# Kernel tuning notes

Hardware: AMD Instinct MI355X
Metric: run time of the kernel (lower is better)

The kernel has to match this reference:

```python
import jax, jax.numpy as jnp
import numpy as np

DIM, E, H, HS = 2048, 8, 1408, 2816
B, S = 4, 2048


def setup_inputs() -> dict:
    key = jax.random.key(0)
    ks = jax.random.split(key, 12)
    sc = 0.02
    return {
        "x": jax.random.normal(ks[0], (B, S, DIM), jnp.float32),
        "gate_w": jax.random.normal(ks[1], (E, DIM), jnp.float32) * sc,
        "gate_b": jnp.zeros((E,), jnp.float32),
        "w1": jax.random.normal(ks[2], (E, H, DIM), jnp.float32) * sc,
        "b1": jnp.zeros((E, H), jnp.float32),
        "w3": jax.random.normal(ks[3], (E, H, DIM), jnp.float32) * sc,
        "b3": jnp.zeros((E, H), jnp.float32),
        "w2": jax.random.normal(ks[4], (E, DIM, H), jnp.float32) * sc,
        "b2": jnp.zeros((E, DIM), jnp.float32),
        "sh_gate": jax.random.normal(ks[5], (HS, DIM), jnp.float32) * sc,
        "sh_up": jax.random.normal(ks[6], (HS, DIM), jnp.float32) * sc,
        "sh_down": jax.random.normal(ks[7], (DIM, HS), jnp.float32) * sc,
        "top_k": 2,
    }


def reference(x, gate_w, gate_b, w1, b1, w3, b3, w2, b2, sh_gate, sh_up, sh_down, top_k):
    shape = x.shape
    xt = x.reshape(-1, DIM)                       # [T, D]
    T = xt.shape[0]

    # Router: softmax -> top-k (bias is None so gathered weights == topk probs)
    logits = xt @ gate_w.T + gate_b               # [T, E]
    scores = jax.nn.softmax(logits, axis=-1)
    topk_w, topk_idx = jax.lax.top_k(scores, top_k)  # [T, K]
    # combine weights per (token, expert); topk indices are distinct per row
    combine = jnp.zeros((T, E), xt.dtype).at[jnp.arange(T)[:, None], topk_idx].add(topk_w)

    # Routed experts: dense batched SwiGLU over all experts, weighted combine.
    g = jax.nn.silu(jnp.einsum("td,ehd->teh", xt, w1) + b1)  # [T, E, H]
    u = jnp.einsum("td,ehd->teh", xt, w3) + b3               # [T, E, H]
    hw = (g * u) * combine[:, :, None]                        # weight before down-proj
    routed = jnp.einsum("teh,edh->td", hw, w2) + combine @ b2  # [T, D]

    # Shared expert (bias-free SwiGLU)
    shared = (jax.nn.silu(xt @ sh_gate.T) * (xt @ sh_up.T)) @ sh_down.T

    return (shared + routed).reshape(shape)
```

## Files before the change

### kernel.cpp

```cpp
#include <hip/hip_runtime.h>
#include <stdint.h>

#define DIM  2048
#define NEXP 8
#define NH   1408
#define NHS  2816
#define NT   8192
#define NA   (NT*2)

typedef unsigned short u16;
typedef short bf16x8 __attribute__((ext_vector_type(8)));
typedef float f32x4 __attribute__((ext_vector_type(4)));

typedef __attribute__((address_space(1))) const uint32_t gas_u32;
typedef __attribute__((address_space(3))) uint32_t las_u32;

__device__ __forceinline__ u16 f2bf(float f) {
  uint32_t x = __builtin_bit_cast(uint32_t, f);
  x += 0x7FFFu + ((x >> 16) & 1u);
  return (u16)(x >> 16);
}

__device__ __forceinline__ void gload_lds16(const void* g, void* l) {
  __builtin_amdgcn_global_load_lds((gas_u32*)g, (las_u32*)l, 16, 0, 0);
}

__device__ __forceinline__ bool xcd_map_band(int G, int& nt, int& mt) {
  const int gx = gridDim.x;
  int f = blockIdx.y * gx + blockIdx.x;
  int xcd = f & 7;
  int local = f >> 3;
  if (G <= 0) return false;
  int band = (G + 7) >> 3;
  int slot = local % band;
  int ntv  = local / band;
  if (ntv >= gx) return false;
  int mtv = xcd * band + slot;
  if (mtv >= G) return false;
  nt = ntv; mt = mtv;
  return true;
}

struct alignas(16) US8 { u16 u[8]; };
struct alignas(8)  US4 { u16 u[4]; };

__global__ __launch_bounds__(256) void convert_kernel(const float* __restrict__ src,
                                                      u16* __restrict__ dst, int n8) {
  int i = blockIdx.x * 256 + threadIdx.x;
  if (i >= n8) return;
  const float4* s = (const float4*)src + (size_t)i * 2;
  float4 a = s[0], b = s[1];
  US8 r;
  r.u[0]=f2bf(a.x); r.u[1]=f2bf(a.y); r.u[2]=f2bf(a.z); r.u[3]=f2bf(a.w);
  r.u[4]=f2bf(b.x); r.u[5]=f2bf(b.y); r.u[6]=f2bf(b.z); r.u[7]=f2bf(b.w);
  *((US8*)dst + i) = r;
}

__global__ void zero_counts(int* counts) { if (threadIdx.x < NEXP) counts[threadIdx.x] = 0; }

__global__ __launch_bounds__(64) void router_kernel(const float* __restrict__ x,
    const float* __restrict__ gw, const float* __restrict__ gb,
    u16* __restrict__ xb,
    int* __restrict__ tope, float* __restrict__ topw, int* __restrict__ counts) {
  const int t = blockIdx.x;
  const int lane = threadIdx.x;
  const float4* xr = (const float4*)(x + (size_t)t * DIM);
  float4 xv[8];
  #pragma unroll
  for (int j = 0; j < 8; j++) xv[j] = xr[j * 64 + lane];
  US4* xrow = (US4*)(xb + (size_t)t * DIM);
  #pragma unroll
  for (int j = 0; j < 8; j++) {
    US4 r4;
    r4.u[0] = f2bf(xv[j].x); r4.u[1] = f2bf(xv[j].y);
    r4.u[2] = f2bf(xv[j].z); r4.u[3] = f2bf(xv[j].w);
    xrow[j * 64 + lane] = r4;
  }
  float p[NEXP];
  #pragma unroll
  for (int e = 0; e < NEXP; e++) {
    const float4* gr = (const float4*)(gw + (size_t)e * DIM);
    float s = 0.f;
    #pragma unroll
    for (int j = 0; j < 8; j++) {
      float4 g = gr[j * 64 + lane];
      s += xv[j].x*g.x + xv[j].y*g.y + xv[j].z*g.z + xv[j].w*g.w;
    }
    p[e] = s;
  }
  #pragma unroll
  for (int off = 32; off > 0; off >>= 1) {
    #pragma unroll
    for (int e = 0; e < NEXP; e++) p[e] += __shfl_xor(p[e], off);
  }
  if (lane == 0) {
    float pr[NEXP];
    float mx = -1e30f;
    #pragma unroll
    for (int e = 0; e < NEXP; e++) { p[e] += gb[e]; mx = fmaxf(mx, p[e]); }
    float den = 0.f;
    #pragma unroll
    for (int e = 0; e < NEXP; e++) { pr[e] = __expf(p[e] - mx); den += pr[e]; }
    float inv = 1.f / den;
    #pragma unroll
    for (int e = 0; e < NEXP; e++) pr[e] *= inv;
    int e0 = 0;
    #pragma unroll
    for (int e = 1; e < NEXP; e++) if (pr[e] > pr[e0]) e0 = e;
    int e1 = (e0 == 0) ? 1 : 0;
    #pragma unroll
    for (int e = 0; e < NEXP; e++) { if (e != e0 && pr[e] > pr[e1]) e1 = e; }
    tope[t*2]   = e0; tope[t*2+1] = e1;
    topw[t*2]   = pr[e0]; topw[t*2+1] = pr[e1];
    atomicAdd(&counts[e0], 1); atomicAdd(&counts[e1], 1);
  }
}

__global__ void scan_kernel(const int* __restrict__ counts, int* __restrict__ offsets,
                            int* __restrict__ cursor) {
  if (threadIdx.x == 0) {
    int s = 0;
    for (int e = 0; e < NEXP; e++) { offsets[e] = s; cursor[e] = s; s += counts[e]; }
    offsets[NEXP] = s;
  }
}

__global__ __launch_bounds__(256) void assign_kernel(const int* __restrict__ tope,
    const float* __restrict__ topw, int* __restrict__ cursor,
    int* __restrict__ ptok, float* __restrict__ pw) {
  int t = blockIdx.x * 256 + threadIdx.x;
  if (t >= NT) return;
  #pragma unroll
  for (int k = 0; k < 2; k++) {
    int e = tope[t*2+k];
    int pos = atomicAdd(&cursor[e], 1);
    ptok[pos] = t;
    pw[pos]   = topw[t*2+k];
  }
}

template<bool ROUTED>
__global__ __launch_bounds__(256, 2) void gemm_up(
    const u16* __restrict__ X,
    const u16* __restrict__ Wg,
    const u16* __restrict__ Wu,
    const float* __restrict__ Bg,
    const float* __restrict__ Bu,
    u16* __restrict__ Hout,
    const int* __restrict__ offsets,
    const int* __restrict__ ptok,
    const float* __restrict__ pw,
    int Nfeat)
{
  int e = 0, seg = 0, cnt = NT;
  if (ROUTED) {
    e = blockIdx.z;
    seg = offsets[e];
    cnt = offsets[e+1] - seg;
  }
  const int G = ROUTED ? ((cnt + 127) >> 7) : (int)gridDim.y;
  int nt, mt;
  if (!xcd_map_band(G, nt, mt)) return;
  const int m0 = mt * 128;
  const int tid = threadIdx.x;
  const int wave = tid >> 6, lane = tid & 63;

  __shared__ u16 sA[128*64];
  __shared__ u16 sBg[64*64];
  __shared__ u16 sBu[64*64];
  char* sAc  = (char*)sA;
  char* sBgc = (char*)sBg;
  char* sBuc = (char*)sBu;

  const u16* aSrc[4];
  #pragma unroll
  for (int j = 0; j < 4; j++) {
    int c = j * 256 + tid;
    int row = c >> 3, gch = (c & 7) ^ (row & 7);
    int r = m0 + row;
    size_t srow;
    if (ROUTED) { r = (r < cnt) ? r : (cnt - 1); srow = (size_t)ptok[seg + r]; }
    else        { srow = (size_t)r; }
    aSrc[j] = X + srow * DIM + gch * 8;
  }
  const size_t wOff = ROUTED ? (size_t)e * Nfeat * DIM : 0;
  const u16 *bgSrc[2], *buSrc[2];
  #pragma unroll
  for (int j = 0; j < 2; j++) {
    int c = j * 256 + tid;
    int row = c >> 3, gch = (c & 7) ^ (row & 7);
    bgSrc[j] = Wg + wOff + (size_t)(nt * 64 + row) * DIM + gch * 8;
    buSrc[j] = Wu + wOff + (size_t)(nt * 64 + row) * DIM + gch * 8;
  }

  f32x4 accg[4][2], accu[4][2];
  #pragma unroll
  for (int m = 0; m < 4; m++)
    #pragma unroll
    for (int n = 0; n < 2; n++) { accg[m][n] = (f32x4){0,0,0,0}; accu[m][n] = (f32x4){0,0,0,0}; }

  const int wr = (wave >> 1) * 64;
  const int wc = (wave & 1) * 32;
  const int lr = lane & 15, kg = lane >> 4;
  int aOff[4], bOff[2];
  #pragma unroll
  for (int m = 0; m < 4; m++) { int row = wr + m*16 + lr; aOff[m] = row*128 + ((kg ^ (row & 7)) & 7) * 16; }
  #pragma unroll
  for (int n = 0; n < 2; n++) { int row = wc + n*16 + lr; bOff[n] = row*128 + ((kg ^ (row & 7)) & 7) * 16; }

  for (int k0 = 0; k0 < DIM; k0 += 64) {
    __syncthreads();
    #pragma unroll
    for (int j = 0; j < 4; j++) gload_lds16(aSrc[j] + k0, sAc + j*4096 + wave*1024);
    #pragma unroll
    for (int j = 0; j < 2; j++) {
      gload_lds16(bgSrc[j] + k0, sBgc + j*4096 + wave*1024);
      gload_lds16(buSrc[j] + k0, sBuc + j*4096 + wave*1024);
    }
    __syncthreads();
    bf16x8 af[4][2], bgf[2][2], buf2[2][2];
    #pragma unroll
    for (int m = 0; m < 4; m++) {
      af[m][0] = *(const bf16x8*)(sAc + aOff[m]);
      af[m][1] = *(const bf16x8*)(sAc + (aOff[m] ^ 64));
    }
    #pragma unroll
    for (int n = 0; n < 2; n++) {
      bgf[n][0]  = *(const bf16x8*)(sBgc + bOff[n]);
      bgf[n][1]  = *(const bf16x8*)(sBgc + (bOff[n] ^ 64));
      buf2[n][0] = *(const bf16x8*)(sBuc + bOff[n]);
      buf2[n][1] = *(const bf16x8*)(sBuc + (bOff[n] ^ 64));
    }
    #pragma unroll
    for (int kk = 0; kk < 2; kk++)
      #pragma unroll
      for (int m = 0; m < 4; m++)
        #pragma unroll
        for (int n = 0; n < 2; n++) {
          accg[m][n] = __builtin_amdgcn_mfma_f32_16x16x32_bf16(af[m][kk], bgf[n][kk],  accg[m][n], 0, 0, 0);
          accu[m][n] = __builtin_amdgcn_mfma_f32_16x16x32_bf16(af[m][kk], buf2[n][kk], accu[m][n], 0, 0, 0);
        }
  }

  const int col0 = nt * 64 + wc;
  #pragma unroll
  for (int m = 0; m < 4; m++) {
    #pragma unroll
    for (int n = 0; n < 2; n++) {
      #pragma unroll
      for (int i = 0; i < 4; i++) {
        int rl = wr + m*16 + (lane >> 4) * 4 + i;
        int gr = m0 + rl;
        if (ROUTED && gr >= cnt) continue;
        int col = col0 + n*16 + (lane & 15);
        float g = accg[m][n][i];
        float u = accu[m][n][i];
        float scale = 1.f;
        size_t orow;
        if (ROUTED) {
          int ai = seg + gr;
          scale = pw[ai];
          g += Bg[e * Nfeat + col];
          u += Bu[e * Nfeat + col];
          orow = (size_t)ai;
        } else {
          orow = (size_t)gr;
        }
        float s = g / (1.f + __expf(-g));
        Hout[orow * (size_t)Nfeat + col] = f2bf(s * u * scale);
      }
    }
  }
}

template<bool ROUTED>
__global__ __launch_bounds__(256, 2) void gemm_down(
    const u16* __restrict__ Hin,
    const u16* __restrict__ W,
    const float* __restrict__ B2,
    float* __restrict__ Out,
    const int* __restrict__ offsets,
    const int* __restrict__ ptok,
    const float* __restrict__ pw,
    int Kdim)
{
  int e = 0, seg = 0, cnt = NT;
  if (ROUTED) {
    e = blockIdx.z;
    seg = offsets[e];
    cnt = offsets[e+1] - seg;
  }
  const int G = ROUTED ? ((cnt + 127) >> 7) : (int)gridDim.y;
  int nt, mt;
  if (!xcd_map_band(G, nt, mt)) return;
  const int m0 = mt * 128;
  const int tid = threadIdx.x;
  const int wave = tid >> 6, lane = tid & 63;

  __shared__ u16 sA[128*64];
  __shared__ u16 sB[128*64];
  char* sAc = (char*)sA;
  char* sBc = (char*)sB;

  const u16* aSrc[4]; const u16* bSrc[4];
  #pragma unroll
  for (int j = 0; j < 4; j++) {
    int c = j * 256 + tid;
    int row = c >> 3, gch = (c & 7) ^ (row & 7);
    int r = m0 + row;
    size_t arow;
    if (ROUTED) { r = (r < cnt) ? r : (cnt - 1); arow = (size_t)(seg + r); }
    else        { arow = (size_t)r; }
    aSrc[j] = Hin + arow * (size_t)Kdim + gch * 8;
    size_t brow = (size_t)(ROUTED ? e * DIM : 0) + nt * 128 + row;
    bSrc[j] = W + brow * (size_t)Kdim + gch * 8;
  }

  f32x4 acc[4][4];
  #pragma unroll
  for (int m = 0; m < 4; m++)
    #pragma unroll
    for (int n = 0; n < 4; n++) acc[m][n] = (f32x4){0,0,0,0};

  const int wr = (wave >> 1) * 64, wc = (wave & 1) * 64;
  const int lr = lane & 15, kg = lane >> 4;
  int aOff[4], bOff[4];
  #pragma unroll
  for (int m = 0; m < 4; m++) { int row = wr + m*16 + lr; aOff[m] = row*128 + ((kg ^ (row & 7)) & 7) * 16; }
  #pragma unroll
  for (int n = 0; n < 4; n++) { int row = wc + n*16 + lr; bOff[n] = row*128 + ((kg ^ (row & 7)) & 7) * 16; }

  for (int k0 = 0; k0 < Kdim; k0 += 64) {
    __syncthreads();
    #pragma unroll
    for (int j = 0; j < 4; j++) {
      gload_lds16(aSrc[j] + k0, sAc + j*4096 + wave*1024);
      gload_lds16(bSrc[j] + k0, sBc + j*4096 + wave*1024);
    }
    __syncthreads();
    bf16x8 af[4][2], bf[4][2];
    #pragma unroll
    for (int m = 0; m < 4; m++) {
      af[m][0] = *(const bf16x8*)(sAc + aOff[m]);
      af[m][1] = *(const bf16x8*)(sAc + (aOff[m] ^ 64));
    }
    #pragma unroll
    for (int n = 0; n < 4; n++) {
      bf[n][0] = *(const bf16x8*)(sBc + bOff[n]);
      bf[n][1] = *(const bf16x8*)(sBc + (bOff[n] ^ 64));
    }
    #pragma unroll
    for (int kk = 0; kk < 2; kk++)
      #pragma unroll
      for (int m = 0; m < 4; m++)
        #pragma unroll
        for (int n = 0; n < 4; n++)
          acc[m][n] = __builtin_amdgcn_mfma_f32_16x16x32_bf16(af[m][kk], bf[n][kk], acc[m][n], 0, 0, 0);
  }

  const int col0 = nt * 128 + wc;
  #pragma unroll
  for (int m = 0; m < 4; m++) {
    #pragma unroll
    for (int n = 0; n < 4; n++) {
      #pragma unroll
      for (int i = 0; i < 4; i++) {
        int rl = wr + m*16 + (lane >> 4) * 4 + i;
        int gr = m0 + rl;
        int col = col0 + n*16 + (lane & 15);
        float v = acc[m][n][i];
        if (ROUTED) {
          if (gr < cnt) {
            int ai = seg + gr;
            int token = ptok[ai];
            float w = pw[ai];
            atomicAdd(Out + (size_t)token * DIM + col, v + w * B2[e * DIM + col]);
          }
        } else {
          Out[(size_t)gr * DIM + col] = v;
        }
      }
    }
  }
}

extern "C" void kernel_launch(void* const* d_in, const int* in_sizes, int n_in,
                              void* d_out, int out_size, void* d_ws, size_t ws_size,
                              hipStream_t stream) {
  (void)in_sizes; (void)n_in; (void)out_size; (void)ws_size;
  const float* x      = (const float*)d_in[0];
  const float* gate_w = (const float*)d_in[1];
  const float* gate_b = (const float*)d_in[2];
  const float* w1     = (const float*)d_in[3];
  const float* b1     = (const float*)d_in[4];
  const float* w3     = (const float*)d_in[5];
  const float* b3     = (const float*)d_in[6];
  const float* w2     = (const float*)d_in[7];
  const float* b2     = (const float*)d_in[8];
  const float* shg    = (const float*)d_in[9];
  const float* shu    = (const float*)d_in[10];
  const float* shd    = (const float*)d_in[11];
  float* out = (float*)d_out;

  char* ws = (char*)d_ws;
  size_t off = 0;
  auto alloc = [&](size_t bytes) -> void* {
    void* p = ws + off;
    off += (bytes + 255) & ~(size_t)255;
    return p;
  };
  u16* xb    = (u16*)alloc((size_t)NT * DIM * 2);
  u16* w1b   = (u16*)alloc((size_t)NEXP * NH * DIM * 2);
  u16* w3b   = (u16*)alloc((size_t)NEXP * NH * DIM * 2);
  u16* w2b   = (u16*)alloc((size_t)NEXP * DIM * NH * 2);
  u16* shgb  = (u16*)alloc((size_t)NHS * DIM * 2);
  u16* shub  = (u16*)alloc((size_t)NHS * DIM * 2);
  u16* shdb  = (u16*)alloc((size_t)DIM * NHS * 2);
  u16* hsh   = (u16*)alloc((size_t)NT * NHS * 2);
  u16* hr    = (u16*)alloc((size_t)NA * NH * 2);
  int*   tope    = (int*)alloc(NT * 2 * 4);
  float* topw    = (float*)alloc(NT * 2 * 4);
  int*   ptok    = (int*)alloc(NA * 4);
  float* pw      = (float*)alloc(NA * 4);
  int*   counts  = (int*)alloc(64);
  int*   offsets = (int*)alloc(64);
  int*   cursor  = (int*)alloc(64);

  auto cvt = [&](const float* s, u16* d, size_t n) {
    int n8 = (int)(n / 8);
    convert_kernel<<<(n8 + 255) / 256, 256, 0, stream>>>(s, d, n8);
  };
  cvt(w1,  w1b,  (size_t)NEXP * NH * DIM);
  cvt(w3,  w3b,  (size_t)NEXP * NH * DIM);
  cvt(w2,  w2b,  (size_t)NEXP * DIM * NH);
  cvt(shg, shgb, (size_t)NHS * DIM);
  cvt(shu, shub, (size_t)NHS * DIM);
  cvt(shd, shdb, (size_t)DIM * NHS);

  zero_counts<<<1, 64, 0, stream>>>(counts);
  router_kernel<<<NT, 64, 0, stream>>>(x, gate_w, gate_b, xb, tope, topw, counts);
  scan_kernel<<<1, 1, 0, stream>>>(counts, offsets, cursor);
  assign_kernel<<<NT / 256, 256, 0, stream>>>(tope, topw, cursor, ptok, pw);

  gemm_up<false><<<dim3(NHS / 64, NT / 128, 1), 256, 0, stream>>>(
      xb, shgb, shub, nullptr, nullptr, hsh, nullptr, nullptr, nullptr, NHS);
  gemm_up<true><<<dim3(NH / 64, NT / 128, NEXP), 256, 0, stream>>>(
      xb, w1b, w3b, b1, b3, hr, offsets, ptok, pw, NH);
  gemm_down<false><<<dim3(DIM / 128, NT / 128, 1), 256, 0, stream>>>(
      hsh, shdb, nullptr, out, nullptr, nullptr, nullptr, NHS);
  gemm_down<true><<<dim3(DIM / 128, NT / 128, NEXP), 256, 0, stream>>>(
      hr, w2b, b2, out, offsets, ptok, pw, NH);
}
```

Measured before the change: 1.106 ms.

## Split routed slots by top-k rank to replace atomics with plain read-modify-write

Routed assignments are now bucketed by (expert, k-rank), so within each rank a token appears at most once. The routed down-projection runs as two launches, one per rank, and each does a plain read-add-write to the output instead of an atomicAdd. The up-projection grid grows to 16 segments, which splits each expert's rows into two buckets and can leave more partially filled 128-row tiles. Correctness depends on the two launches running in order on the same stream, which they do.

```diff
diff --git a/kernel.cpp b/kernel.cpp
--- a/kernel.cpp
+++ b/kernel.cpp
@@ -7,6 +7,7 @@
 #define NHS  2816
 #define NT   8192
 #define NA   (NT*2)
+#define NV   (NEXP*2)
 
 typedef unsigned short u16;
 typedef short bf16x8 __attribute__((ext_vector_type(8)));
@@ -56,7 +57,7 @@
   *((US8*)dst + i) = r;
 }
 
-__global__ void zero_counts(int* counts) { if (threadIdx.x < NEXP) counts[threadIdx.x] = 0; }
+__global__ void zero_counts(int* counts) { if (threadIdx.x < NV) counts[threadIdx.x] = 0; }
 
 __global__ __launch_bounds__(64) void router_kernel(const float* __restrict__ x,
     const float* __restrict__ gw, const float* __restrict__ gb,
@@ -112,7 +113,7 @@
     for (int e = 0; e < NEXP; e++) { if (e != e0 && pr[e] > pr[e1]) e1 = e; }
     tope[t*2]   = e0; tope[t*2+1] = e1;
     topw[t*2]   = pr[e0]; topw[t*2+1] = pr[e1];
-    atomicAdd(&counts[e0], 1); atomicAdd(&counts[e1], 1);
+    atomicAdd(&counts[e0*2+0], 1); atomicAdd(&counts[e1*2+1], 1);
   }
 }
 
@@ -120,8 +121,8 @@
                             int* __restrict__ cursor) {
   if (threadIdx.x == 0) {
     int s = 0;
-    for (int e = 0; e < NEXP; e++) { offsets[e] = s; cursor[e] = s; s += counts[e]; }
-    offsets[NEXP] = s;
+    for (int v = 0; v < NV; v++) { offsets[v] = s; cursor[v] = s; s += counts[v]; }
+    offsets[NV] = s;
   }
 }
 
@@ -132,8 +133,8 @@
   if (t >= NT) return;
   #pragma unroll
   for (int k = 0; k < 2; k++) {
-    int e = tope[t*2+k];
-    int pos = atomicAdd(&cursor[e], 1);
+    int v = tope[t*2+k] * 2 + k;
+    int pos = atomicAdd(&cursor[v], 1);
     ptok[pos] = t;
     pw[pos]   = topw[t*2+k];
   }
@@ -141,22 +142,18 @@
 
 template<bool ROUTED>
 __global__ __launch_bounds__(256, 2) void gemm_up(
-    const u16* __restrict__ X,
-    const u16* __restrict__ Wg,
-    const u16* __restrict__ Wu,
-    const float* __restrict__ Bg,
-    const float* __restrict__ Bu,
+    const u16* __restrict__ X, const u16* __restrict__ Wg, const u16* __restrict__ Wu,
+    const float* __restrict__ Bg, const float* __restrict__ Bu,
     u16* __restrict__ Hout,
-    const int* __restrict__ offsets,
-    const int* __restrict__ ptok,
-    const float* __restrict__ pw,
-    int Nfeat)
+    const int* __restrict__ offsets, const int* __restrict__ ptok,
+    const float* __restrict__ pw, int Nfeat)
 {
   int e = 0, seg = 0, cnt = NT;
   if (ROUTED) {
-    e = blockIdx.z;
-    seg = offsets[e];
-    cnt = offsets[e+1] - seg;
+    int v = blockIdx.z;
+    e = v >> 1;
+    seg = offsets[v];
+    cnt = offsets[v+1] - seg;
   }
   const int G = ROUTED ? ((cnt + 127) >> 7) : (int)gridDim.y;
   int nt, mt;
@@ -275,20 +272,17 @@
 
 template<bool ROUTED>
 __global__ __launch_bounds__(256, 2) void gemm_down(
-    const u16* __restrict__ Hin,
-    const u16* __restrict__ W,
-    const float* __restrict__ B2,
-    float* __restrict__ Out,
-    const int* __restrict__ offsets,
-    const int* __restrict__ ptok,
-    const float* __restrict__ pw,
-    int Kdim)
+    const u16* __restrict__ Hin, const u16* __restrict__ W,
+    const float* __restrict__ B2, float* __restrict__ Out,
+    const int* __restrict__ offsets, const int* __restrict__ ptok,
+    const float* __restrict__ pw, int Kdim, int kpar)
 {
   int e = 0, seg = 0, cnt = NT;
   if (ROUTED) {
     e = blockIdx.z;
-    seg = offsets[e];
-    cnt = offsets[e+1] - seg;
+    int v = e * 2 + kpar;
+    seg = offsets[v];
+    cnt = offsets[v+1] - seg;
   }
   const int G = ROUTED ? ((cnt + 127) >> 7) : (int)gridDim.y;
   int nt, mt;
@@ -374,7 +368,8 @@
             int ai = seg + gr;
             int token = ptok[ai];
             float w = pw[ai];
-            atomicAdd(Out + (size_t)token * DIM + col, v + w * B2[e * DIM + col]);
+            float* p = Out + (size_t)token * DIM + col;
+            *p = *p + v + w * B2[e * DIM + col];
           }
         } else {
           Out[(size_t)gr * DIM + col] = v;
@@ -422,9 +417,9 @@
   float* topw    = (float*)alloc(NT * 2 * 4);
   int*   ptok    = (int*)alloc(NA * 4);
   float* pw      = (float*)alloc(NA * 4);
-  int*   counts  = (int*)alloc(64);
-  int*   offsets = (int*)alloc(64);
-  int*   cursor  = (int*)alloc(64);
+  int*   counts  = (int*)alloc(256);
+  int*   offsets = (int*)alloc(256);
+  int*   cursor  = (int*)alloc(256);
 
   auto cvt = [&](const float* s, u16* d, size_t n) {
     int n8 = (int)(n / 8);
@@ -444,10 +439,12 @@
 
   gemm_up<false><<<dim3(NHS / 64, NT / 128, 1), 256, 0, stream>>>(
       xb, shgb, shub, nullptr, nullptr, hsh, nullptr, nullptr, nullptr, NHS);
-  gemm_up<true><<<dim3(NH / 64, NT / 128, NEXP), 256, 0, stream>>>(
+  gemm_up<true><<<dim3(NH / 64, NT / 128, NV), 256, 0, stream>>>(
       xb, w1b, w3b, b1, b3, hr, offsets, ptok, pw, NH);
   gemm_down<false><<<dim3(DIM / 128, NT / 128, 1), 256, 0, stream>>>(
-      hsh, shdb, nullptr, out, nullptr, nullptr, nullptr, NHS);
+      hsh, shdb, nullptr, out, nullptr, nullptr, nullptr, NHS, 0);
   gemm_down<true><<<dim3(DIM / 128, NT / 128, NEXP), 256, 0, stream>>>(
-      hr, w2b, b2, out, offsets, ptok, pw, NH);
-}
+      hr, w2b, b2, out, offsets, ptok, pw, NH, 0);
+  gemm_down<true><<<dim3(DIM / 128, NT / 128, NEXP), 256, 0, stream>>>(
+      hr, w2b, b2, out, offsets, ptok, pw, NH, 1);
+}
```

Measured after the change: 1.264 ms. 14.3% more time.
